# Kernel tuning notes

Measured on AMD Instinct MI355X. Metric: run time of the kernel, lower is better.

Reference implementation:

```python
import jax, jax.numpy as jnp
import numpy as np

B, SQ, SK = 8, 128, 128
IVD, DIM, EV, H, NH = 32, 32, 64, 8, 128
DK = EV // H


def setup_inputs() -> dict:
    key = jax.random.key(0)
    ks = jax.random.split(key, 16)
    n = lambda k, s: jax.random.normal(k, s, dtype=jnp.float32)
    lin = lambda k, fi, fo: n(k, (fi, fo)) / np.float32(np.sqrt(fi))
    d = {}
    d['query_value'] = n(ks[0], (B, SQ, IVD))
    d['key_value']   = n(ks[1], (B, SK, IVD))
    d['value']       = n(ks[2], (B, SK, DIM))
    d['impute_data'] = n(ks[3], (B, SQ, IVD // 2))
    d['emb_mask'] = jax.random.randint(ks[4], (B, SK, DIM), 0, 2).astype(jnp.int32)
    # learn_value_embedding: Linear(IVD,NH)+Tanh+Linear(NH,EV,no bias)
    d['w1'] = lin(ks[5], IVD, NH); d['b1'] = jnp.zeros((NH,), jnp.float32)
    d['w2'] = lin(ks[6], NH, EV)
    # linears[0], linears[1]: Linear(EV,EV)
    d['wq'] = lin(ks[7], EV, EV); d['bq'] = jnp.zeros((EV,), jnp.float32)
    d['wk'] = lin(ks[8], EV, EV); d['bk'] = jnp.zeros((EV,), jnp.float32)
    # linears[2]: Linear(DIM*H, NH)
    d['wo'] = lin(ks[9], DIM * H, NH); d['bo'] = jnp.zeros((NH,), jnp.float32)
    # query_data_enc: Linear(IVD/2,NH)+LayerNorm(NH)+ReLU+Linear(NH,NH)
    d['wd1'] = lin(ks[10], IVD // 2, NH); d['bd1'] = jnp.zeros((NH,), jnp.float32)
    d['ln_g'] = jnp.ones((NH,), jnp.float32); d['ln_b'] = jnp.zeros((NH,), jnp.float32)
    d['wd2'] = lin(ks[11], NH, NH); d['bd2'] = jnp.zeros((NH,), jnp.float32)
    return d


def reference(query_value, key_value, value, impute_data,
              w1, b1, w2, wq, bq, wk, bk, wo, bo,
              wd1, bd1, ln_g, ln_b, wd2, bd2, emb_mask):
    b = query_value.shape[0]
    dim = value.shape[-1]
    # value embeddings: Linear -> Tanh -> Linear(no bias)
    qe = jnp.tanh(query_value @ w1 + b1) @ w2   # [B,Sq,EV]
    ke = jnp.tanh(key_value @ w1 + b1) @ w2     # [B,Sk,EV]
    q = (qe @ wq + bq).reshape(b, -1, H, DK).transpose(0, 2, 1, 3)  # [B,H,Sq,DK]
    k = (ke @ wk + bk).reshape(b, -1, H, DK).transpose(0, 2, 1, 3)  # [B,H,Sk,DK]
    scores = jnp.einsum('bhqd,bhkd->bhqk', q, k) / np.float32(np.sqrt(DK))
    # broadcast scores over the value channel dim; masked_fill with -10000
    m = emb_mask[:, None, None, :, :]           # [B,1,1,Sk,dim]
    logits = jnp.where(m == 0, jnp.float32(-10000.0), scores[..., None])  # [B,H,Sq,Sk,dim]
    p_attn = jax.nn.softmax(logits, axis=-2)    # softmax over Sk per channel
    out = jnp.einsum('bhqkd,bkd->bhqd', p_attn, value)  # [B,H,Sq,dim]
    x = out.transpose(0, 2, 1, 3).reshape(b, -1, H * dim)
    y = x @ wo + bo                             # [B,Sq,NH]
    # query_data_enc branch
    h1 = impute_data @ wd1 + bd1
    mu = jnp.mean(h1, axis=-1, keepdims=True)
    var = jnp.var(h1, axis=-1, keepdims=True)
    ln = (h1 - mu) / jnp.sqrt(var + 1e-5) * ln_g + ln_b
    query_data = jax.nn.relu(ln) @ wd2 + bd2    # [B,Sq,NH]
    return y, query_data
```

## Files before the change

### kernel.cpp

```cpp
#include <hip/hip_runtime.h>
#include <math.h>

#define B 8
#define SQ 128
#define SK 128
#define IVD 32
#define DIM 32
#define EV 64
#define H 8
#define NH 128
#define DK 8
#define TQ 2
#define PAD 132

__global__ __launch_bounds__(128) void fused1_kernel(
    const float* __restrict__ qv, const float* __restrict__ kv,
    const float* __restrict__ w1, const float* __restrict__ b1,
    const float* __restrict__ w2,
    const float* __restrict__ wq, const float* __restrict__ bqv,
    const float* __restrict__ wk, const float* __restrict__ bkv,
    float* __restrict__ qout, float* __restrict__ kout,
    const float* __restrict__ imp,
    const float* __restrict__ wd1, const float* __restrict__ bd1,
    const float* __restrict__ ln_g, const float* __restrict__ ln_b,
    const float* __restrict__ wd2, const float* __restrict__ bd2,
    float* __restrict__ qd)
{
    const int r = blockIdx.x;
    const int tid = threadIdx.x;

    if (r < 2 * B * SQ) {
        __shared__ float xs[IVD];
        __shared__ float h1[NH];
        __shared__ float ev[EV];
        __shared__ float part[128];
        const float* src; const float* wp; const float* bp; float* dst;
        if (r < B * SQ) {
            src = qv + r * IVD; wp = wq; bp = bqv; dst = qout + r * EV;
        } else {
            const int rr = r - B * SQ;
            src = kv + rr * IVD; wp = wk; bp = bkv; dst = kout + rr * EV;
        }
        if (tid < IVD) xs[tid] = src[tid];
        __syncthreads();
        float acc = b1[tid];
        #pragma unroll
        for (int i = 0; i < IVD; ++i) acc += xs[i] * w1[i * NH + tid];
        h1[tid] = tanhf(acc);
        __syncthreads();

        const int o = tid & 63, hf = tid >> 6;
        {
            float a = 0.f;
            const float* w2p = w2 + o;
            #pragma unroll 8
            for (int i = hf * 64; i < hf * 64 + 64; ++i) a += h1[i] * w2p[i * EV];
            part[tid] = a;
        }
        __syncthreads();
        if (tid < EV) ev[tid] = part[tid] + part[tid + 64];
        __syncthreads();
        {
            float a = 0.f;
            const float* wpp = wp + o;
            #pragma unroll 8
            for (int j = hf * 32; j < hf * 32 + 32; ++j) a += ev[j] * wpp[j * EV];
            part[tid] = a;
        }
        __syncthreads();
        if (tid < EV) dst[tid] = part[tid] + part[tid + 64] + bp[tid];
    } else {
        const int bs = r - 2 * B * SQ;
        __shared__ float xs2[IVD / 2];
        __shared__ float h1b[NH];
        __shared__ float red[2];

        if (tid < IVD / 2) xs2[tid] = imp[bs * (IVD / 2) + tid];
        __syncthreads();
        float acc = bd1[tid];
        #pragma unroll
        for (int i = 0; i < IVD / 2; ++i) acc += xs2[i] * wd1[i * NH + tid];

        float s = acc;
        #pragma unroll
        for (int off = 32; off > 0; off >>= 1) s += __shfl_down(s, off, 64);
        if ((tid & 63) == 0) red[tid >> 6] = s;
        __syncthreads();
        const float mean = (red[0] + red[1]) * (1.f / NH);
        const float diff = acc - mean;
        float s2 = diff * diff;
        __syncthreads();
        #pragma unroll
        for (int off = 32; off > 0; off >>= 1) s2 += __shfl_down(s2, off, 64);
        if ((tid & 63) == 0) red[tid >> 6] = s2;
        __syncthreads();
        const float var = (red[0] + red[1]) * (1.f / NH);

        const float ln = diff * rsqrtf(var + 1e-5f) * ln_g[tid] + ln_b[tid];
        h1b[tid] = fmaxf(ln, 0.f);
        __syncthreads();

        float a = bd2[tid];
        #pragma unroll 8
        for (int j = 0; j < NH; ++j) a += h1b[j] * wd2[j * NH + tid];
        qd[bs * NH + tid] = a;
    }
}

__global__ __launch_bounds__(256) void attn_kernel(
    const float* __restrict__ qproj, const float* __restrict__ kproj,
    const float* __restrict__ value, const int* __restrict__ mask,
    const float* __restrict__ wo, const float* __restrict__ bo,
    float* __restrict__ y)
{
    const int blk = blockIdx.x;
    const int b = blk >> 6;
    const int q0 = (blk & 63) * TQ;
    const int tid = threadIdx.x;

    __shared__ __align__(16) float qs[TQ * EV];
    __shared__ __align__(16) float sc[TQ * H * SK];
    __shared__ __align__(16) float mvt[DIM * PAD];
    __shared__ __align__(16) float mmt[DIM * PAD];
    __shared__ __align__(16) float xr[TQ * H * DIM];
    __shared__ __align__(16) float ypart[2 * TQ * NH];
    __shared__ float hmax[TQ * H];

    if (tid < TQ * EV) qs[tid] = qproj[(b * SQ + q0) * EV + tid];
    for (int idx = tid; idx < SK * DIM; idx += 256) {
        const int k = idx >> 5, d = idx & 31;
        const float v = value[b * SK * DIM + idx];
        const float m = (float)mask[b * SK * DIM + idx];
        mvt[d * PAD + k] = v * m;
        mmt[d * PAD + k] = m;
    }
    __syncthreads();

    #pragma unroll
    for (int i = 0; i < (TQ * H * SK) / 256; ++i) {
        const int p = tid + i * 256;
        const int q = p >> 10, rem = p & 1023, h = rem >> 7, k = rem & 127;
        const float* kr = kproj + (b * SK + k) * EV + h * DK;
        const float* qq = qs + q * EV + h * DK;
        float dsum = 0.f;
        #pragma unroll
        for (int j = 0; j < DK; ++j) dsum += qq[j] * kr[j];
        sc[p] = dsum * 0.3535533905932738f;
    }
    __syncthreads();

    {
        const int grp = tid >> 4, ln = tid & 15;
        float m = -1e30f;
        #pragma unroll
        for (int j = 0; j < 8; ++j) m = fmaxf(m, sc[(grp << 7) + ln * 8 + j]);
        #pragma unroll
        for (int off = 8; off; off >>= 1) m = fmaxf(m, __shfl_down(m, off, 16));
        if (ln == 0) hmax[grp] = m;
    }
    __syncthreads();
    {
        const int grp = tid >> 4, ln = tid & 15;
        const float hm = hmax[grp];
        #pragma unroll
        for (int j = 0; j < 8; ++j) {
            const int idx = (grp << 7) + ln * 8 + j;
            sc[idx] = __expf(sc[idx] - hm);
        }
    }
    __syncthreads();

    {
        const int h = tid >> 5, d = tid & 31;
        const float4* vp = (const float4*)&mvt[d * PAD];
        const float4* mp = (const float4*)&mmt[d * PAD];
        #pragma unroll
        for (int q = 0; q < TQ; ++q) {
            const float4* sp = (const float4*)&sc[(q * H + h) * SK];
            float num = 0.f, den = 0.f;
            #pragma unroll 8
            for (int k4 = 0; k4 < SK / 4; ++k4) {
                const float4 s = sp[k4], v = vp[k4], m = mp[k4];
                num += s.x * v.x + s.y * v.y + s.z * v.z + s.w * v.w;
                den += s.x * m.x + s.y * m.y + s.z * m.z + s.w * m.w;
            }
            xr[q * (H * DIM) + h * DIM + d] = num / den;
        }
    }
    __syncthreads();

    {
        const int n = tid & 127, half = tid >> 7;
        const float* wop = wo + half * 128 * NH + n;
        const float* x0 = xr + half * 128;
        const float* x1 = xr + (H * DIM) + half * 128;
        float a0 = 0.f, a1 = 0.f;
        #pragma unroll 4
        for (int j = 0; j < 128; ++j) {
            const float w = wop[j * NH];
            a0 += w * x0[j];
            a1 += w * x1[j];
        }
        ypart[half * (TQ * NH) + 0 * NH + n] = a0;
        ypart[half * (TQ * NH) + 1 * NH + n] = a1;
    }
    __syncthreads();
    {
        const int q = tid >> 7, n = tid & 127;
        y[(b * SQ + q0 + q) * NH + n] =
            ypart[q * NH + n] + ypart[TQ * NH + q * NH + n] + bo[n];
    }
}

extern "C" void kernel_launch(void* const* d_in, const int* in_sizes, int n_in,
                              void* d_out, int out_size, void* d_ws, size_t ws_size,
                              hipStream_t stream) {
    const float* query_value = (const float*)d_in[0];
    const float* key_value   = (const float*)d_in[1];
    const float* value       = (const float*)d_in[2];
    const float* impute      = (const float*)d_in[3];
    const int*   emb_mask    = (const int*)d_in[4];
    const float* w1   = (const float*)d_in[5];
    const float* b1   = (const float*)d_in[6];
    const float* w2   = (const float*)d_in[7];
    const float* wq   = (const float*)d_in[8];
    const float* bq   = (const float*)d_in[9];
    const float* wk   = (const float*)d_in[10];
    const float* bk   = (const float*)d_in[11];
    const float* wo   = (const float*)d_in[12];
    const float* bo   = (const float*)d_in[13];
    const float* wd1  = (const float*)d_in[14];
    const float* bd1  = (const float*)d_in[15];
    const float* ln_g = (const float*)d_in[16];
    const float* ln_b = (const float*)d_in[17];
    const float* wd2  = (const float*)d_in[18];
    const float* bd2  = (const float*)d_in[19];

    float* y  = (float*)d_out;
    float* qd = y + B * SQ * NH;

    float* qproj = (float*)d_ws;
    float* kproj = qproj + B * SQ * EV;

    hipLaunchKernelGGL(fused1_kernel, dim3(3 * B * SQ), dim3(128), 0, stream,
                       query_value, key_value, w1, b1, w2, wq, bq, wk, bk,
                       qproj, kproj,
                       impute, wd1, bd1, ln_g, ln_b, wd2, bd2, qd);
    hipLaunchKernelGGL(attn_kernel, dim3(B * SQ / TQ), dim3(256), 0, stream,
                       qproj, kproj, value, emb_mask, wo, bo, y);
}
```

Baseline: 117.3 us.

## Process two rows per block, drop softmax max pass, split attention reduction over key groups

The projection and LayerNorm kernel now handles two rows per block, so each weight load is reused twice and the grid is half the size. tanhf is replaced by a clamped exp-based tanh. The attention kernel folds the score scale into q, exponentiates scores directly without subtracting the row max, and vectorises the q·k dot with float4 loads. The numerator and denominator sums are split across 8 key groups whose per-thread value and mask registers are reused across heads, then reduced through shared memory. Skipping the max subtraction risks overflow for large scores, and the new reduction adds extra shared memory and barriers.

After: 114.8 us. 2.1% less time.

```diff
diff --git a/kernel.cpp b/kernel.cpp
--- a/kernel.cpp
+++ b/kernel.cpp
@@ -11,7 +11,14 @@
 #define NH 128
 #define DK 8
 #define TQ 2
+#define KG 8
 #define PAD 132
+
+__device__ __forceinline__ float fast_tanh(float x) {
+    const float xc = fminf(fmaxf(x, -10.f), 10.f);
+    const float t = __expf(2.f * xc);
+    return (t - 1.f) / (t + 1.f);
+}
 
 __global__ __launch_bounds__(128) void fused1_kernel(
     const float* __restrict__ qv, const float* __restrict__ kv,
@@ -29,81 +36,112 @@
     const int r = blockIdx.x;
     const int tid = threadIdx.x;
 
-    if (r < 2 * B * SQ) {
-        __shared__ float xs[IVD];
-        __shared__ float h1[NH];
-        __shared__ float ev[EV];
-        __shared__ float part[128];
+    if (r < 1024) {
+        __shared__ float xs[2][IVD];
+        __shared__ float h1[2][NH];
+        __shared__ float ev[2][EV];
+        __shared__ float part[2][128];
         const float* src; const float* wp; const float* bp; float* dst;
-        if (r < B * SQ) {
-            src = qv + r * IVD; wp = wq; bp = bqv; dst = qout + r * EV;
-        } else {
-            const int rr = r - B * SQ;
-            src = kv + rr * IVD; wp = wk; bp = bkv; dst = kout + rr * EV;
-        }
-        if (tid < IVD) xs[tid] = src[tid];
-        __syncthreads();
-        float acc = b1[tid];
-        #pragma unroll
-        for (int i = 0; i < IVD; ++i) acc += xs[i] * w1[i * NH + tid];
-        h1[tid] = tanhf(acc);
+        int row0;
+        if (r < 512) { row0 = r * 2;         src = qv; wp = wq; bp = bqv; dst = qout; }
+        else         { row0 = (r - 512) * 2; src = kv; wp = wk; bp = bkv; dst = kout; }
+
+        if (tid < 2 * IVD) xs[tid >> 5][tid & 31] = src[row0 * IVD + tid];
+        __syncthreads();
+
+        {
+            float a0 = b1[tid], a1 = a0;
+            #pragma unroll
+            for (int i = 0; i < IVD; ++i) {
+                const float w = w1[i * NH + tid];
+                a0 += xs[0][i] * w; a1 += xs[1][i] * w;
+            }
+            h1[0][tid] = fast_tanh(a0);
+            h1[1][tid] = fast_tanh(a1);
+        }
         __syncthreads();
 
         const int o = tid & 63, hf = tid >> 6;
         {
-            float a = 0.f;
-            const float* w2p = w2 + o;
+            float c0 = 0.f, c1 = 0.f;
             #pragma unroll 8
-            for (int i = hf * 64; i < hf * 64 + 64; ++i) a += h1[i] * w2p[i * EV];
-            part[tid] = a;
-        }
-        __syncthreads();
-        if (tid < EV) ev[tid] = part[tid] + part[tid + 64];
-        __syncthreads();
-        {
-            float a = 0.f;
-            const float* wpp = wp + o;
+            for (int i = hf * 64; i < hf * 64 + 64; ++i) {
+                const float w = w2[i * EV + o];
+                c0 += h1[0][i] * w; c1 += h1[1][i] * w;
+            }
+            part[0][tid] = c0; part[1][tid] = c1;
+        }
+        __syncthreads();
+        {
+            const int row = tid >> 6, oo = tid & 63;
+            ev[row][oo] = part[row][oo] + part[row][oo + 64];
+        }
+        __syncthreads();
+        {
+            float c0 = 0.f, c1 = 0.f;
             #pragma unroll 8
-            for (int j = hf * 32; j < hf * 32 + 32; ++j) a += ev[j] * wpp[j * EV];
-            part[tid] = a;
-        }
-        __syncthreads();
-        if (tid < EV) dst[tid] = part[tid] + part[tid + 64] + bp[tid];
+            for (int j = hf * 32; j < hf * 32 + 32; ++j) {
+                const float w = wp[j * EV + o];
+                c0 += ev[0][j] * w; c1 += ev[1][j] * w;
+            }
+            part[0][tid] = c0; part[1][tid] = c1;
+        }
+        __syncthreads();
+        {
+            const int row = tid >> 6, oo = tid & 63;
+            dst[(row0 + row) * EV + oo] = part[row][oo] + part[row][oo + 64] + bp[oo];
+        }
     } else {
-        const int bs = r - 2 * B * SQ;
-        __shared__ float xs2[IVD / 2];
-        __shared__ float h1b[NH];
-        __shared__ float red[2];
-
-        if (tid < IVD / 2) xs2[tid] = imp[bs * (IVD / 2) + tid];
-        __syncthreads();
-        float acc = bd1[tid];
-        #pragma unroll
-        for (int i = 0; i < IVD / 2; ++i) acc += xs2[i] * wd1[i * NH + tid];
-
-        float s = acc;
-        #pragma unroll
-        for (int off = 32; off > 0; off >>= 1) s += __shfl_down(s, off, 64);
-        if ((tid & 63) == 0) red[tid >> 6] = s;
-        __syncthreads();
-        const float mean = (red[0] + red[1]) * (1.f / NH);
-        const float diff = acc - mean;
-        float s2 = diff * diff;
-        __syncthreads();
-        #pragma unroll
-        for (int off = 32; off > 0; off >>= 1) s2 += __shfl_down(s2, off, 64);
-        if ((tid & 63) == 0) red[tid >> 6] = s2;
-        __syncthreads();
-        const float var = (red[0] + red[1]) * (1.f / NH);
-
-        const float ln = diff * rsqrtf(var + 1e-5f) * ln_g[tid] + ln_b[tid];
-        h1b[tid] = fmaxf(ln, 0.f);
-        __syncthreads();
-
-        float a = bd2[tid];
+        const int bs0 = (r - 1024) * 2;
+        __shared__ float xs2[2][IVD / 2];
+        __shared__ float h1b[2][NH];
+        __shared__ float red[2][2];
+
+        if (tid < IVD) xs2[tid >> 4][tid & 15] = imp[bs0 * (IVD / 2) + tid];
+        __syncthreads();
+        float a0 = bd1[tid], a1 = a0;
+        #pragma unroll
+        for (int i = 0; i < IVD / 2; ++i) {
+            const float w = wd1[i * NH + tid];
+            a0 += xs2[0][i] * w; a1 += xs2[1][i] * w;
+        }
+
+        float s0 = a0, s1 = a1;
+        #pragma unroll
+        for (int off = 32; off > 0; off >>= 1) {
+            s0 += __shfl_down(s0, off, 64);
+            s1 += __shfl_down(s1, off, 64);
+        }
+        if ((tid & 63) == 0) { red[0][tid >> 6] = s0; red[1][tid >> 6] = s1; }
+        __syncthreads();
+        const float mu0 = (red[0][0] + red[0][1]) * (1.f / NH);
+        const float mu1 = (red[1][0] + red[1][1]) * (1.f / NH);
+        const float d0 = a0 - mu0, d1 = a1 - mu1;
+        float t0 = d0 * d0, t1 = d1 * d1;
+        __syncthreads();
+        #pragma unroll
+        for (int off = 32; off > 0; off >>= 1) {
+            t0 += __shfl_down(t0, off, 64);
+            t1 += __shfl_down(t1, off, 64);
+        }
+        if ((tid & 63) == 0) { red[0][tid >> 6] = t0; red[1][tid >> 6] = t1; }
+        __syncthreads();
+        const float v0 = (red[0][0] + red[0][1]) * (1.f / NH);
+        const float v1 = (red[1][0] + red[1][1]) * (1.f / NH);
+
+        const float g = ln_g[tid], bb = ln_b[tid];
+        h1b[0][tid] = fmaxf(d0 * rsqrtf(v0 + 1e-5f) * g + bb, 0.f);
+        h1b[1][tid] = fmaxf(d1 * rsqrtf(v1 + 1e-5f) * g + bb, 0.f);
+        __syncthreads();
+
+        float c0 = bd2[tid], c1 = c0;
         #pragma unroll 8
-        for (int j = 0; j < NH; ++j) a += h1b[j] * wd2[j * NH + tid];
-        qd[bs * NH + tid] = a;
+        for (int j = 0; j < NH; ++j) {
+            const float w = wd2[j * NH + tid];
+            c0 += h1b[0][j] * w; c1 += h1b[1][j] * w;
+        }
+        qd[bs0 * NH + tid] = c0;
+        qd[(bs0 + 1) * NH + tid] = c1;
     }
 }
 
@@ -122,11 +160,11 @@
     __shared__ __align__(16) float sc[TQ * H * SK];
     __shared__ __align__(16) float mvt[DIM * PAD];
     __shared__ __align__(16) float mmt[DIM * PAD];
+    __shared__ __align__(16) float2 part[H * KG * DIM];
     __shared__ __align__(16) float xr[TQ * H * DIM];
     __shared__ __align__(16) float ypart[2 * TQ * NH];
-    __shared__ float hmax[TQ * H];
-
-    if (tid < TQ * EV) qs[tid] = qproj[(b * SQ + q0) * EV + tid];
+
+    if (tid < TQ * EV) qs[tid] = qproj[(b * SQ + q0) * EV + tid] * 0.3535533905932738f;
     for (int idx = tid; idx < SK * DIM; idx += 256) {
         const int k = idx >> 5, d = idx & 31;
         const float v = value[b * SK * DIM + idx];
@@ -140,54 +178,51 @@
     for (int i = 0; i < (TQ * H * SK) / 256; ++i) {
         const int p = tid + i * 256;
         const int q = p >> 10, rem = p & 1023, h = rem >> 7, k = rem & 127;
-        const float* kr = kproj + (b * SK + k) * EV + h * DK;
-        const float* qq = qs + q * EV + h * DK;
-        float dsum = 0.f;
-        #pragma unroll
-        for (int j = 0; j < DK; ++j) dsum += qq[j] * kr[j];
-        sc[p] = dsum * 0.3535533905932738f;
+        const float4* kr = (const float4*)(kproj + (b * SK + k) * EV + h * DK);
+        const float4* qq = (const float4*)(qs + q * EV + h * DK);
+        const float4 k0 = kr[0], k1 = kr[1], qa = qq[0], qb = qq[1];
+        const float s = qa.x * k0.x + qa.y * k0.y + qa.z * k0.z + qa.w * k0.w
+                      + qb.x * k1.x + qb.y * k1.y + qb.z * k1.z + qb.w * k1.w;
+        sc[p] = __expf(s);
     }
     __syncthreads();
 
     {
-        const int grp = tid >> 4, ln = tid & 15;
-        float m = -1e30f;
-        #pragma unroll
-        for (int j = 0; j < 8; ++j) m = fmaxf(m, sc[(grp << 7) + ln * 8 + j]);
-        #pragma unroll
-        for (int off = 8; off; off >>= 1) m = fmaxf(m, __shfl_down(m, off, 16));
-        if (ln == 0) hmax[grp] = m;
-    }
-    __syncthreads();
-    {
-        const int grp = tid >> 4, ln = tid & 15;
-        const float hm = hmax[grp];
-        #pragma unroll
-        for (int j = 0; j < 8; ++j) {
-            const int idx = (grp << 7) + ln * 8 + j;
-            sc[idx] = __expf(sc[idx] - hm);
-        }
-    }
-    __syncthreads();
-
-    {
-        const int h = tid >> 5, d = tid & 31;
-        const float4* vp = (const float4*)&mvt[d * PAD];
-        const float4* mp = (const float4*)&mmt[d * PAD];
+        const int d = tid & 31, kg = tid >> 5;
+        float4 vv[4], mq[4];
+        const float4* vp = (const float4*)&mvt[d * PAD + kg * 16];
+        const float4* mp = (const float4*)&mmt[d * PAD + kg * 16];
+        #pragma unroll
+        for (int j = 0; j < 4; ++j) { vv[j] = vp[j]; mq[j] = mp[j]; }
+
         #pragma unroll
         for (int q = 0; q < TQ; ++q) {
-            const float4* sp = (const float4*)&sc[(q * H + h) * SK];
-            float num = 0.f, den = 0.f;
-            #pragma unroll 8
-            for (int k4 = 0; k4 < SK / 4; ++k4) {
-                const float4 s = sp[k4], v = vp[k4], m = mp[k4];
-                num += s.x * v.x + s.y * v.y + s.z * v.z + s.w * v.w;
-                den += s.x * m.x + s.y * m.y + s.z * m.z + s.w * m.w;
-            }
-            xr[q * (H * DIM) + h * DIM + d] = num / den;
-        }
-    }
-    __syncthreads();
+            #pragma unroll
+            for (int h = 0; h < H; ++h) {
+                const float4* sp = (const float4*)&sc[(q * H + h) * SK + kg * 16];
+                float num = 0.f, den = 0.f;
+                #pragma unroll
+                for (int j = 0; j < 4; ++j) {
+                    const float4 s = sp[j];
+                    num += s.x * vv[j].x + s.y * vv[j].y + s.z * vv[j].z + s.w * vv[j].w;
+                    den += s.x * mq[j].x + s.y * mq[j].y + s.z * mq[j].z + s.w * mq[j].w;
+                }
+                part[(h * KG + kg) * DIM + d] = make_float2(num, den);
+            }
+            __syncthreads();
+            {
+                const int h = tid >> 5;
+                float num = 0.f, den = 0.f;
+                #pragma unroll
+                for (int g = 0; g < KG; ++g) {
+                    const float2 p2 = part[(h * KG + g) * DIM + d];
+                    num += p2.x; den += p2.y;
+                }
+                xr[q * (H * DIM) + tid] = num / den;
+            }
+            __syncthreads();
+        }
+    }
 
     {
         const int n = tid & 127, half = tid >> 7;
@@ -242,7 +277,7 @@
     float* qproj = (float*)d_ws;
     float* kproj = qproj + B * SQ * EV;
 
-    hipLaunchKernelGGL(fused1_kernel, dim3(3 * B * SQ), dim3(128), 0, stream,
+    hipLaunchKernelGGL(fused1_kernel, dim3(1536), dim3(128), 0, stream,
                        query_value, key_value, w1, b1, w2, wq, bq, wk, bk,
                        qproj, kproj,
                        impute, wd1, bd1, ln_g, ln_b, wd2, bd2, qd);
```
